# Kernel optimization log

Hardware: AMD Instinct MI355X
Metric: run time of the kernel (lower is better)

The kernel has to match this reference:

```python
import jax, jax.numpy as jnp
import numpy as np

D = 512
HEADS, DIM_HEAD, LANDMARKS, PINV_ITERS = 8, 64, 256, 6
CONV_K = 33  # residual depthwise conv kernel over sequence dim


def _ln(x, g, b, eps=1e-5):
    mu = x.mean(-1, keepdims=True)
    var = ((x - mu) ** 2).mean(-1, keepdims=True)
    return (x - mu) / jnp.sqrt(var + eps) * g + b


def _moe(x, gw, gb, f1w, f1b, l1g, l1b, f2w, f2b, l2g, l2b, k):
    # Dense grouped-expert evaluation (same math as per-token dispatch in torch source).
    scores = x @ gw + gb                               # [B,N,E]
    topk_s, topk_i = jax.lax.top_k(scores, k)          # [B,N,k]
    h = jnp.einsum('bnd,edh->benh', x, f1w) + f1b[None, :, None, :]
    h = jax.nn.relu(_ln(h, l1g[None, :, None, :], l1b[None, :, None, :]))
    o = jnp.einsum('benh,ehd->bend', h, f2w) + f2b[None, :, None, :]
    o = _ln(o, l2g[None, :, None, :], l2b[None, :, None, :])  # [B,E,N,D]
    o = jnp.take_along_axis(jnp.swapaxes(o, 1, 2), topk_i[..., None], axis=2)  # [B,N,k,D]
    w = jax.nn.softmax(topk_s, axis=-1)[..., None]
    return (w * o).sum(axis=2) + x


def _pinv(x, iters):
    # Moore-Penrose iterative pseudoinverse (lucidrains nystrom-attention)
    col = jnp.abs(x).sum(-1).max()
    row = jnp.abs(x).sum(-2).max()
    z = jnp.swapaxes(x, -1, -2) / (col * row)
    I = jnp.eye(x.shape[-1], dtype=x.dtype)
    for _ in range(iters):
        xz = x @ z
        z = 0.25 * z @ (13 * I - xz @ (15 * I - xz @ (7 * I - xz)))
    return z


def _nystrom(x, qkv_w, out_w, out_b, conv_w):
    b, n, _ = x.shape
    m, h, dh = LANDMARKS, HEADS, DIM_HEAD
    pad = (m - n % m) % m
    x = jnp.pad(x, ((0, 0), (pad, 0), (0, 0)))  # pad at FRONT, as in source
    npd = n + pad
    qkv = x @ qkv_w                              # [b, npd, 3*h*dh]
    q, k, v = [t.reshape(b, npd, h, dh).transpose(0, 2, 1, 3) for t in jnp.split(qkv, 3, axis=-1)]
    q = q * dh ** -0.5
    l = npd // m
    q_l = q.reshape(b, h, m, l, dh).mean(3)      # landmark means
    k_l = k.reshape(b, h, m, l, dh).mean(3)
    attn1 = jax.nn.softmax(jnp.einsum('bhid,bhjd->bhij', q, k_l), -1)    # [b,h,npd,m]
    attn2 = jax.nn.softmax(jnp.einsum('bhid,bhjd->bhij', q_l, k_l), -1)  # [b,h,m,m]
    attn3 = jax.nn.softmax(jnp.einsum('bhid,bhjd->bhij', q_l, k), -1)    # [b,h,m,npd]
    out = (attn1 @ _pinv(attn2, PINV_ITERS)) @ (attn3 @ v)               # [b,h,npd,dh]
    res = jax.lax.conv_general_dilated(
        v, conv_w, (1, 1), [(CONV_K // 2, CONV_K // 2), (0, 0)],
        dimension_numbers=('NCHW', 'OIHW', 'NCHW'), feature_group_count=h)
    out = out + res
    out = out.transpose(0, 2, 1, 3).reshape(b, npd, h * dh)
    out = out @ out_w + out_b
    return out[:, -n:]


def setup_inputs() -> dict:
    key = jax.random.key(0)
    ks = iter(jax.random.split(key, 64))
    def rn(shape, s=0.02):
        return jax.random.normal(next(ks), shape, jnp.float32) * s
    inp = {'features': jax.random.normal(next(ks), (4, 6000, D), jnp.float32)}
    inp['cls_token'] = rn((1, 1, D), 1e-6)
    def moe_params(pfx, E):
        inp[pfx + '_gate_w'] = rn((D, E)); inp[pfx + '_gate_b'] = jnp.zeros((E,), jnp.float32)
        inp[pfx + '_fc1_w'] = rn((E, D, D)); inp[pfx + '_fc1_b'] = jnp.zeros((E, D), jnp.float32)
        inp[pfx + '_ln1_g'] = jnp.ones((E, D), jnp.float32); inp[pfx + '_ln1_b'] = jnp.zeros((E, D), jnp.float32)
        inp[pfx + '_fc2_w'] = rn((E, D, D)); inp[pfx + '_fc2_b'] = jnp.zeros((E, D), jnp.float32)
        inp[pfx + '_ln2_g'] = jnp.ones((E, D), jnp.float32); inp[pfx + '_ln2_b'] = jnp.zeros((E, D), jnp.float32)
    moe_params('moe1', 2)
    moe_params('moe2', 4)
    def layer_params(pfx):
        inp[pfx + '_norm_g'] = jnp.ones((D,), jnp.float32); inp[pfx + '_norm_b'] = jnp.zeros((D,), jnp.float32)
        inp[pfx + '_qkv_w'] = rn((D, 3 * HEADS * DIM_HEAD))
        inp[pfx + '_out_w'] = rn((HEADS * DIM_HEAD, D)); inp[pfx + '_out_b'] = jnp.zeros((D,), jnp.float32)
        inp[pfx + '_conv_w'] = rn((HEADS, 1, CONV_K, 1))
    layer_params('l1')
    layer_params('l2')
    return inp


def reference(features, cls_token,
              moe1_gate_w, moe1_gate_b, moe1_fc1_w, moe1_fc1_b, moe1_ln1_g, moe1_ln1_b, moe1_fc2_w, moe1_fc2_b, moe1_ln2_g, moe1_ln2_b,
              moe2_gate_w, moe2_gate_b, moe2_fc1_w, moe2_fc1_b, moe2_ln1_g, moe2_ln1_b, moe2_fc2_w, moe2_fc2_b, moe2_ln2_g, moe2_ln2_b,
              l1_norm_g, l1_norm_b, l1_qkv_w, l1_out_w, l1_out_b, l1_conv_w,
              l2_norm_g, l2_norm_b, l2_qkv_w, l2_out_w, l2_out_b, l2_conv_w):
    B, N, _ = features.shape
    _H = int(np.ceil(np.sqrt(N)))
    add = _H * _H - N
    h = jnp.concatenate([features, features[:, :add]], axis=1)      # square pad by wrap
    h = jnp.concatenate([jnp.broadcast_to(cls_token, (B, 1, D)), h], axis=1)
    h = _moe(h, moe1_gate_w, moe1_gate_b, moe1_fc1_w, moe1_fc1_b, moe1_ln1_g, moe1_ln1_b, moe1_fc2_w, moe1_fc2_b, moe1_ln2_g, moe1_ln2_b, k=1)
    h = h + _nystrom(_ln(h, l1_norm_g, l1_norm_b), l1_qkv_w, l1_out_w, l1_out_b, l1_conv_w)
    h = _moe(h, moe2_gate_w, moe2_gate_b, moe2_fc1_w, moe2_fc1_b, moe2_ln1_g, moe2_ln1_b, moe2_fc2_w, moe2_fc2_b, moe2_ln2_g, moe2_ln2_b, k=2)
    h = h + _nystrom(_ln(h, l2_norm_g, l2_norm_b), l2_qkv_w, l2_out_w, l2_out_b, l2_conv_w)
    return (h[:, 0], h[:, 1:])
```

## Files before the change

### kernel.cpp

```cpp
#include <hip/hip_runtime.h>
#include <hip/hip_bf16.h>

constexpr int BATCH = 4;
constexpr int NTOK  = 6085;
constexpr int BN_TOK = BATCH * NTOK;
constexpr int NPD   = 6144;
constexpr int RPAD  = BATCH * NPD;
constexpr int DMODEL = 512;
constexpr int NH = 8, DH = 64;
constexpr int NBH = BATCH * NH;
constexpr int LGRP = NPD / 256;
constexpr int PAD_FRONT = 59;
constexpr int CONVK = 33;
constexpr int NCH = 8;

typedef __attribute__((ext_vector_type(8))) short short8v;
typedef __attribute__((ext_vector_type(4))) float f32x4;

__device__ __forceinline__ unsigned short f2bf(float f) {
  unsigned u = __float_as_uint(f);
  u += 0x7FFF + ((u >> 16) & 1);
  return (unsigned short)(u >> 16);
}
__device__ __forceinline__ float bf2f(unsigned short h) {
  return __uint_as_float((unsigned)h << 16);
}


__global__ void k_build_h(const float* __restrict__ feat, const float* __restrict__ cls,
                          float* __restrict__ H) {
  size_t total = (size_t)BN_TOK * DMODEL;
  for (size_t idx = (size_t)blockIdx.x * blockDim.x + threadIdx.x; idx < total;
       idx += (size_t)gridDim.x * blockDim.x) {
    int d = (int)(idx & 511);
    size_t tok = idx >> 9;
    int b = (int)(tok / NTOK), n = (int)(tok % NTOK);
    float v;
    if (n == 0) v = cls[d];
    else {
      int i = n - 1; if (i >= 6000) i -= 6000;
      v = feat[((size_t)b * 6000 + i) * DMODEL + d];
    }
    H[idx] = v;
  }
}

__global__ void k_diag_fill(float* __restrict__ out, size_t n, float val) {
  for (size_t i = (size_t)blockIdx.x * blockDim.x + threadIdx.x; i < n;
       i += (size_t)gridDim.x * blockDim.x)
    out[i] = val;
}

__global__ __launch_bounds__(256) void k_wconv(const float* __restrict__ W, int ldb,
    unsigned short* __restrict__ hi, unsigned short* __restrict__ lo) {
  __shared__ unsigned short Th[64][80], Tl[64][80];
  int bk = blockIdx.y * 64, bn = blockIdx.x * 64;
  int t = threadIdx.x;
  int kr = t >> 2, cq = (t & 3) * 16;
  const float* src = W + (size_t)(bk + kr) * ldb + bn + cq;
  #pragma unroll
  for (int q = 0; q < 4; ++q) {
    float4 v = *(const float4*)(src + q * 4);
    float vs[4] = {v.x, v.y, v.z, v.w};
    #pragma unroll
    for (int e = 0; e < 4; ++e) {
      int n = cq + q * 4 + e;
      unsigned short h = f2bf(vs[e]);
      Th[n][kr] = h;
      Tl[n][kr] = f2bf(vs[e] - bf2f(h));
    }
  }
  __syncthreads();
  int nr = t >> 2, kq = (t & 3) * 16;
  size_t o = (size_t)(bn + nr) * 512 + bk + kq;
  *(short8v*)&hi[o]     = *(const short8v*)&Th[nr][kq];
  *(short8v*)&hi[o + 8] = *(const short8v*)&Th[nr][kq + 8];
  *(short8v*)&lo[o]     = *(const short8v*)&Tl[nr][kq];
  *(short8v*)&lo[o + 8] = *(const short8v*)&Tl[nr][kq + 8];
}

__global__ __launch_bounds__(256) void k_gemm_mfma(const float* __restrict__ A,
    const unsigned short* __restrict__ BtH, const unsigned short* __restrict__ BtL,
    const float* __restrict__ bias, float* __restrict__ C,
    int M, int lda, int ldc, float alpha, int omode, unsigned short* __restrict__ Clo)
{
  __shared__ unsigned short AsH[128][40], AsL[128][40];
  __shared__ unsigned short BsH[128][40], BsL[128][40];
  int bm = blockIdx.y * 128, bn = blockIdx.x * 128;
  int tid = threadIdx.x;
  int wave = tid >> 6, lane = tid & 63;
  int mo = (wave >> 1) * 64, no = (wave & 1) * 64;
  int r16 = lane & 15, g = lane >> 4;
  f32x4 acc[4][4] = {};
  int srow = tid >> 1, shalf = (tid & 1) * 16;
  const float* aptr = A + (size_t)(bm + srow) * lda + shalf;
  bool avalid = (bm + srow) < M;
  const unsigned short* bhptr = BtH + (size_t)(bn + srow) * 512 + shalf;
  const unsigned short* blptr = BtL + (size_t)(bn + srow) * 512 + shalf;
  for (int k0 = 0; k0 < 512; k0 += 32) {
    unsigned short h8[16], l8[16];
    #pragma unroll
    for (int q = 0; q < 4; ++q) {
      float4 v = avalid ? *(const float4*)(aptr + k0 + q * 4) : make_float4(0.f, 0.f, 0.f, 0.f);
      float vs[4] = {v.x, v.y, v.z, v.w};
      #pragma unroll
      for (int e = 0; e < 4; ++e) {
        unsigned short hh = f2bf(vs[e]);
        h8[q * 4 + e] = hh;
        l8[q * 4 + e] = f2bf(vs[e] - bf2f(hh));
      }
    }
    *(short8v*)&AsH[srow][shalf]     = *(short8v*)&h8[0];
    *(short8v*)&AsH[srow][shalf + 8] = *(short8v*)&h8[8];
    *(short8v*)&AsL[srow][shalf]     = *(short8v*)&l8[0];
    *(short8v*)&AsL[srow][shalf + 8] = *(short8v*)&l8[8];
    *(short8v*)&BsH[srow][shalf]     = *(const short8v*)(bhptr + k0);
    *(short8v*)&BsH[srow][shalf + 8] = *(const short8v*)(bhptr + k0 + 8);
    *(short8v*)&BsL[srow][shalf]     = *(const short8v*)(blptr + k0);
    *(short8v*)&BsL[srow][shalf + 8] = *(const short8v*)(blptr + k0 + 8);
    __syncthreads();
    short8v ah[4], al[4], bh[4], bl[4];
    #pragma unroll
    for (int mt = 0; mt < 4; ++mt) {
      ah[mt] = *(const short8v*)&AsH[mo + mt * 16 + r16][g * 8];
      al[mt] = *(const short8v*)&AsL[mo + mt * 16 + r16][g * 8];
    }
    #pragma unroll
    for (int nt = 0; nt < 4; ++nt) {
      bh[nt] = *(const short8v*)&BsH[no + nt * 16 + r16][g * 8];
      bl[nt] = *(const short8v*)&BsL[no + nt * 16 + r16][g * 8];
    }
    #pragma unroll
    for (int mt = 0; mt < 4; ++mt)
      #pragma unroll
      for (int nt = 0; nt < 4; ++nt) {
        acc[mt][nt] = __builtin_amdgcn_mfma_f32_16x16x32_bf16(ah[mt], bh[nt], acc[mt][nt], 0, 0, 0);
        acc[mt][nt] = __builtin_amdgcn_mfma_f32_16x16x32_bf16(ah[mt], bl[nt], acc[mt][nt], 0, 0, 0);
        acc[mt][nt] = __builtin_amdgcn_mfma_f32_16x16x32_bf16(al[mt], bh[nt], acc[mt][nt], 0, 0, 0);
      }
    __syncthreads();
  }
  #pragma unroll
  for (int mt = 0; mt < 4; ++mt)
    #pragma unroll
    for (int nt = 0; nt < 4; ++nt)
      #pragma unroll
      for (int j = 0; j < 4; ++j) {
        int gr = bm + mo + mt * 16 + g * 4 + j;
        int gc = bn + no + nt * 16 + r16;
        if (gr >= M) continue;
        float v = alpha * acc[mt][nt][j] + (bias ? bias[gc] : 0.f);
        if (omode == 0) {
          C[(size_t)gr * ldc + gc] = v;
        } else if (omode == 2) {
          int bb = gr / NPD, ii = gr % NPD;
          if (ii >= PAD_FRONT)
            C[((size_t)bb * NTOK + ii - PAD_FRONT) * 512 + gc] += v;
        } else if (omode == 3) {
          int bb = gr / NPD, ii = gr % NPD;
          int hh = gc >> 6, dd = gc & 63;
          C[(((size_t)bb * NH + hh) * NPD + ii) * 64 + dd] = v;
        } else {
          int bb = gr / NPD, ii = gr % NPD;
          int hh = gc >> 6, dd = gc & 63;
          size_t idx = (((size_t)bb * NH + hh) * NPD + ii) * 64 + dd;
          unsigned short hi = f2bf(v);
          ((unsigned short*)C)[idx] = hi;
          Clo[idx] = f2bf(v - bf2f(hi));
        }
      }
}

__global__ __launch_bounds__(256) void k_gemm_mfma2(const float* __restrict__ A,
    const float* __restrict__ Bt, float* __restrict__ C,
    float alpha, int omode, float cdiag, int premap, int nprod)
{
  __shared__ unsigned short AsH[128][40], AsL[128][40];
  __shared__ unsigned short BsH[128][40], BsL[128][40];
  size_t zo = (size_t)blockIdx.z * 65536;
  int bm = blockIdx.y * 128, bn = blockIdx.x * 128;
  int tid = threadIdx.x;
  int wave = tid >> 6, lane = tid & 63;
  int mo = (wave >> 1) * 64, no = (wave & 1) * 64;
  int r16 = lane & 15, g = lane >> 4;
  f32x4 acc[4][4] = {};
  int srow = tid >> 1, shalf = (tid & 1) * 16;
  int grow = bm + srow;
  int gn = bn + srow;
  for (int k0 = 0; k0 < 256; k0 += 32) {
    unsigned short h8[16], l8[16];
    #pragma unroll
    for (int q = 0; q < 4; ++q) {
      float4 v = *(const float4*)&A[zo + (size_t)grow * 256 + k0 + shalf + q * 4];
      float vs[4] = {v.x, v.y, v.z, v.w};
      #pragma unroll
      for (int e = 0; e < 4; ++e) {
        float a = vs[e];
        if (premap) a = ((grow == (k0 + shalf + q * 4 + e)) ? 7.f : 0.f) - a;
        unsigned short hh = f2bf(a);
        h8[q * 4 + e] = hh;
        l8[q * 4 + e] = (nprod == 3) ? f2bf(a - bf2f(hh)) : (unsigned short)0;
      }
    }
    *(short8v*)&AsH[srow][shalf]     = *(short8v*)&h8[0];
    *(short8v*)&AsH[srow][shalf + 8] = *(short8v*)&h8[8];
    *(short8v*)&AsL[srow][shalf]     = *(short8v*)&l8[0];
    *(short8v*)&AsL[srow][shalf + 8] = *(short8v*)&l8[8];
    #pragma unroll
    for (int q = 0; q < 4; ++q) {
      float4 v = *(const float4*)&Bt[zo + (size_t)gn * 256 + k0 + shalf + q * 4];
      float vs[4] = {v.x, v.y, v.z, v.w};
      #pragma unroll
      for (int e = 0; e < 4; ++e) {
        unsigned short hh = f2bf(vs[e]);
        h8[q * 4 + e] = hh;
        l8[q * 4 + e] = (nprod == 3) ? f2bf(vs[e] - bf2f(hh)) : (unsigned short)0;
      }
    }
    *(short8v*)&BsH[srow][shalf]     = *(short8v*)&h8[0];
    *(short8v*)&BsH[srow][shalf + 8] = *(short8v*)&h8[8];
    *(short8v*)&BsL[srow][shalf]     = *(short8v*)&l8[0];
    *(short8v*)&BsL[srow][shalf + 8] = *(short8v*)&l8[8];
    __syncthreads();
    short8v ah[4], al[4], bh[4], bl[4];
    #pragma unroll
    for (int mt = 0; mt < 4; ++mt) {
      ah[mt] = *(const short8v*)&AsH[mo + mt * 16 + r16][g * 8];
      al[mt] = *(const short8v*)&AsL[mo + mt * 16 + r16][g * 8];
    }
    #pragma unroll
    for (int nt = 0; nt < 4; ++nt) {
      bh[nt] = *(const short8v*)&BsH[no + nt * 16 + r16][g * 8];
      bl[nt] = *(const short8v*)&BsL[no + nt * 16 + r16][g * 8];
    }
    #pragma unroll
    for (int mt = 0; mt < 4; ++mt)
      #pragma unroll
      for (int nt = 0; nt < 4; ++nt) {
        acc[mt][nt] = __builtin_amdgcn_mfma_f32_16x16x32_bf16(ah[mt], bh[nt], acc[mt][nt], 0, 0, 0);
        if (nprod == 3) {
          acc[mt][nt] = __builtin_amdgcn_mfma_f32_16x16x32_bf16(ah[mt], bl[nt], acc[mt][nt], 0, 0, 0);
          acc[mt][nt] = __builtin_amdgcn_mfma_f32_16x16x32_bf16(al[mt], bh[nt], acc[mt][nt], 0, 0, 0);
        }
      }
    __syncthreads();
  }
  #pragma unroll
  for (int mt = 0; mt < 4; ++mt)
    #pragma unroll
    for (int nt = 0; nt < 4; ++nt)
      #pragma unroll
      for (int j = 0; j < 4; ++j) {
        int gr = bm + mo + mt * 16 + g * 4 + j;
        int gc = bn + no + nt * 16 + r16;
        float v;
        if (omode == 5) v = ((gr == gc) ? cdiag : 0.f) - acc[mt][nt][j];
        else            v = alpha * acc[mt][nt][j];
        C[zo + (size_t)gr * 256 + gc] = v;
      }
}

__global__ __launch_bounds__(256) void k_tpose(const float* __restrict__ in,
                                               float* __restrict__ out) {
  __shared__ float Ts[64][65];
  int bx = blockIdx.x * 64, by = blockIdx.y * 64;
  size_t zo = (size_t)blockIdx.z * 65536;
  int t = threadIdx.x;
  int r = t >> 4, c4 = (t & 15) * 4;
  #pragma unroll
  for (int u = 0; u < 4; ++u) {
    float4 v = *(const float4*)&in[zo + (size_t)(by + r + u * 16) * 256 + bx + c4];
    Ts[r + u * 16][c4 + 0] = v.x; Ts[r + u * 16][c4 + 1] = v.y;
    Ts[r + u * 16][c4 + 2] = v.z; Ts[r + u * 16][c4 + 3] = v.w;
  }
  __syncthreads();
  #pragma unroll
  for (int u = 0; u < 4; ++u) {
    int rr = r + u * 16;
    float4 v = make_float4(Ts[c4][rr], Ts[c4 + 1][rr], Ts[c4 + 2][rr], Ts[c4 + 3][rr]);
    *(float4*)&out[zo + (size_t)(bx + rr) * 256 + by + c4] = v;
  }
}

__global__ void k_y0(const float* __restrict__ A2, float* __restrict__ Y,
                     const unsigned int* __restrict__ sc) {
  float scale = 1.f / (__uint_as_float(sc[0]) * __uint_as_float(sc[1]));
  size_t total = (size_t)NBH * 65536;
  for (size_t idx = (size_t)blockIdx.x * blockDim.x + threadIdx.x; idx < total;
       idx += (size_t)gridDim.x * blockDim.x)
    Y[idx] = A2[idx] * scale;
}

__global__ void k_zinit(const float* __restrict__ A2, float* __restrict__ Z,
                        const unsigned int* __restrict__ sc) {
  float scale = 1.f / (__uint_as_float(sc[0]) * __uint_as_float(sc[1]));
  size_t total = (size_t)NBH * 65536;
  for (size_t idx = (size_t)blockIdx.x * blockDim.x + threadIdx.x; idx < total;
       idx += (size_t)gridDim.x * blockDim.x) {
    size_t bh = idx >> 16; int r = (int)((idx >> 8) & 255); int cc = (int)(idx & 255);
    Z[idx] = A2[(bh << 16) + (size_t)cc * 256 + r] * scale;
  }
}

__global__ __launch_bounds__(256) void k_gemm(const float* __restrict__ A,
    const float* __restrict__ B,
    const float* __restrict__ bias, float* __restrict__ C,
    int M, int N, int K, int lda, int ldb, int ldc,
    long long sA, long long sB, long long sC, float alpha, int omode, float cdiag)
{
  __shared__ float As[16][65];
  __shared__ float Bs[16][65];
  int z = blockIdx.z;
  A += (size_t)z * (size_t)sA;
  B += (size_t)z * (size_t)sB;
  int bm = blockIdx.y * 64, bn = blockIdx.x * 64;
  int tid = threadIdx.x;
  int tr = tid >> 4, tc = tid & 15;
  int ar = tid >> 2, aq = tid & 3;
  int br = tid >> 4, bq = tid & 15;
  float acc[4][4] = {};
  for (int k0 = 0; k0 < K; k0 += 16) {
    {
      int gr = bm + ar;
      float4 v = make_float4(0.f, 0.f, 0.f, 0.f);
      if (gr < M) v = *(const float4*)&A[(size_t)gr * lda + k0 + aq * 4];
      As[aq * 4 + 0][ar] = v.x; As[aq * 4 + 1][ar] = v.y;
      As[aq * 4 + 2][ar] = v.z; As[aq * 4 + 3][ar] = v.w;
    }
    {
      float4 v = *(const float4*)&B[(size_t)(k0 + br) * ldb + bn + bq * 4];
      Bs[br][bq * 4 + 0] = v.x; Bs[br][bq * 4 + 1] = v.y;
      Bs[br][bq * 4 + 2] = v.z; Bs[br][bq * 4 + 3] = v.w;
    }
    __syncthreads();
    #pragma unroll
    for (int kk = 0; kk < 16; ++kk) {
      float a[4], bv[4];
      #pragma unroll
      for (int i = 0; i < 4; ++i) a[i] = As[kk][tr * 4 + i];
      #pragma unroll
      for (int j = 0; j < 4; ++j) bv[j] = Bs[kk][tc * 4 + j];
      #pragma unroll
      for (int i = 0; i < 4; ++i)
        #pragma unroll
        for (int j = 0; j < 4; ++j) acc[i][j] += a[i] * bv[j];
    }
    __syncthreads();
  }
  #pragma unroll
  for (int i = 0; i < 4; ++i) {
    int gr = bm + tr * 4 + i;
    if (gr >= M) continue;
    #pragma unroll
    for (int j = 0; j < 4; ++j) {
      int gc = bn + tc * 4 + j;
      float v;
      if (omode == 5) {
        v = ((gr == gc) ? cdiag : 0.f) - acc[i][j];
      } else {
        v = alpha * acc[i][j] + (bias ? bias[gc] : 0.f);
      }
      C[(size_t)z * (size_t)sC + (size_t)gr * ldc + gc] = v;
    }
  }
}

__global__ void k_gate(const float* __restrict__ X, const float* __restrict__ gw,
                       const float* __restrict__ gb, float* __restrict__ WT, int E, int k) {
  int tok = blockIdx.x; int lane = threadIdx.x;
  const float* x = X + (size_t)tok * DMODEL;
  float s[4] = {0.f, 0.f, 0.f, 0.f};
  for (int d = lane; d < DMODEL; d += 64) {
    float xv = x[d];
    for (int e = 0; e < E; ++e) s[e] += xv * gw[(size_t)d * E + e];
  }
  #pragma unroll
  for (int off = 32; off; off >>= 1) {
    #pragma unroll
    for (int e = 0; e < 4; ++e) s[e] += __shfl_down(s[e], off);
  }
  if (lane == 0) {
    for (int e = 0; e < E; ++e) s[e] += gb[e];
    float w[4] = {0.f, 0.f, 0.f, 0.f};
    int i1 = 0;
    for (int e = 1; e < E; ++e) if (s[e] > s[i1]) i1 = e;
    if (k == 1) {
      w[i1] = 1.f;
    } else {
      int i2 = -1;
      for (int e = 0; e < E; ++e) { if (e == i1) continue; if (i2 < 0 || s[e] > s[i2]) i2 = e; }
      float e2 = expf(s[i2] - s[i1]);
      float zz = 1.f + e2;
      w[i1] = 1.f / zz; w[i2] = e2 / zz;
    }
    #pragma unroll
    for (int e = 0; e < 4; ++e) WT[(size_t)tok * 4 + e] = w[e];
  }
}

__device__ __forceinline__ void wave_ln_stats(const float* x, int lane, float& mu, float& rstd) {
  float s = 0.f, q = 0.f;
  #pragma unroll
  for (int j = 0; j < 8; ++j) { float v = x[lane + 64 * j]; s += v; q += v * v; }
  #pragma unroll
  for (int off = 32; off; off >>= 1) { s += __shfl_xor(s, off); q += __shfl_xor(q, off); }
  mu = s * (1.f / 512.f);
  float var = q * (1.f / 512.f) - mu * mu;
  rstd = rsqrtf(var + 1e-5f);
}

__global__ void k_ln_relu(float* __restrict__ T, const float* __restrict__ g,
                          const float* __restrict__ b) {
  int row = blockIdx.x; int lane = threadIdx.x;
  float* x = T + (size_t)row * 512;
  float mu, rstd; wave_ln_stats(x, lane, mu, rstd);
  #pragma unroll
  for (int j = 0; j < 8; ++j) {
    int d = lane + 64 * j;
    float v = (x[d] - mu) * rstd * g[d] + b[d];
    x[d] = fmaxf(v, 0.f);
  }
}

__global__ void k_ln_waccum(const float* __restrict__ T, float* __restrict__ H,
                            const float* __restrict__ g, const float* __restrict__ b,
                            const float* __restrict__ WT, int e) {
  int row = blockIdx.x;
  float w = WT[(size_t)row * 4 + e];
  if (w == 0.f) return;
  int lane = threadIdx.x;
  const float* x = T + (size_t)row * 512;
  float mu, rstd; wave_ln_stats(x, lane, mu, rstd);
  float* h = H + (size_t)row * 512;
  #pragma unroll
  for (int j = 0; j < 8; ++j) {
    int d = lane + 64 * j;
    h[d] += w * ((x[d] - mu) * rstd * g[d] + b[d]);
  }
}

__global__ void k_ln_pad(const float* __restrict__ H, float* __restrict__ XLn,
                         const float* __restrict__ g, const float* __restrict__ b) {
  int row = blockIdx.x; int lane = threadIdx.x;
  int bb = row / NPD, i = row % NPD;
  float* y = XLn + (size_t)row * 512;
  if (i < PAD_FRONT) {
    #pragma unroll
    for (int j = 0; j < 8; ++j) y[lane + 64 * j] = 0.f;
    return;
  }
  const float* x = H + ((size_t)bb * NTOK + (i - PAD_FRONT)) * 512;
  float mu, rstd; wave_ln_stats(x, lane, mu, rstd);
  #pragma unroll
  for (int j = 0; j < 8; ++j) {
    int d = lane + 64 * j;
    y[d] = (x[d] - mu) * rstd * g[d] + b[d];
  }
}

__global__ void k_xmean(const float* __restrict__ XLn, float* __restrict__ Xm) {
  int z = blockIdx.x;
  int c = threadIdx.x;
  int b = z >> 8, jm = z & 255;
  const float* base = XLn + ((size_t)b * NPD + jm * LGRP) * 512 + c;
  float s = 0.f;
  #pragma unroll
  for (int t = 0; t < LGRP; ++t) s += base[(size_t)t * 512];
  Xm[(size_t)z * 512 + c] = s * (1.f / LGRP);
}

__global__ __launch_bounds__(256) void k_attn2(const float* __restrict__ QL,
                                               const float* __restrict__ KL,
                                               float* __restrict__ A2) {
  int z = blockIdx.x; int bh = z >> 8, j = z & 255;
  int b = bh >> 3, h = bh & 7;
  int t = threadIdx.x;
  __shared__ float q[64]; __shared__ float red[256];
  __shared__ float mshare, sshare;
  if (t < 64) q[t] = QL[((size_t)b * 256 + j) * 512 + h * 64 + t];
  __syncthreads();
  const float* kl = KL + ((size_t)b * 256 + t) * 512 + h * 64;
  float s = 0.f;
  #pragma unroll
  for (int d = 0; d < 64; ++d) s += q[d] * kl[d];
  red[t] = s; __syncthreads();
  for (int st = 128; st; st >>= 1) { if (t < st) red[t] = fmaxf(red[t], red[t + st]); __syncthreads(); }
  if (t == 0) mshare = red[0];
  __syncthreads();
  float e = expf(s - mshare);
  red[t] = e; __syncthreads();
  for (int st = 128; st; st >>= 1) { if (t < st) red[t] += red[t + st]; __syncthreads(); }
  if (t == 0) sshare = red[0];
  __syncthreads();
  A2[((size_t)bh * 256 + j) * 256 + t] = e / sshare;
}

__global__ __launch_bounds__(256) void k_pinv_scalars(const float* __restrict__ A2,
                                                      unsigned int* __restrict__ sc) {
  int bh = blockIdx.x; int t = threadIdx.x;
  const float* A = A2 + (size_t)bh * 65536;
  float rowsum = 0.f, colsum = 0.f;
  for (int jj = 0; jj < 256; ++jj) {
    rowsum += fabsf(A[(size_t)t * 256 + jj]);
    colsum += fabsf(A[(size_t)jj * 256 + t]);
  }
  __shared__ float sh[256];
  sh[t] = rowsum; __syncthreads();
  for (int s = 128; s; s >>= 1) { if (t < s) sh[t] = fmaxf(sh[t], sh[t + s]); __syncthreads(); }
  if (t == 0) atomicMax(&sc[0], __float_as_uint(sh[0]));
  __syncthreads();
  sh[t] = colsum; __syncthreads();
  for (int s = 128; s; s >>= 1) { if (t < s) sh[t] = fmaxf(sh[t], sh[t + s]); __syncthreads(); }
  if (t == 0) atomicMax(&sc[1], __float_as_uint(sh[0]));
}

__global__ __launch_bounds__(256) void k_vtpose(const unsigned short* __restrict__ VrH,
    const unsigned short* __restrict__ VrL,
    unsigned short* __restrict__ VtH, unsigned short* __restrict__ VtL) {
  __shared__ unsigned short TH[64][72], TL[64][72];
  int i0 = blockIdx.x * 64, bh = blockIdx.y;
  int t = threadIdx.x;
  const unsigned short* sH = VrH + ((size_t)bh * NPD + i0) * 64;
  const unsigned short* sL = VrL + ((size_t)bh * NPD + i0) * 64;
  #pragma unroll
  for (int u = 0; u < 2; ++u) {
    int idx = t + 256 * u;
    int r = idx >> 3, c8 = (idx & 7) * 8;
    *(short8v*)&TH[r][c8] = *(const short8v*)&sH[idx * 8];
    *(short8v*)&TL[r][c8] = *(const short8v*)&sL[idx * 8];
  }
  __syncthreads();
  #pragma unroll
  for (int u = 0; u < 2; ++u) {
    int idx = t + 256 * u;
    int d = idx >> 3, c8 = (idx & 7) * 8;
    unsigned short h8[8], l8[8];
    #pragma unroll
    for (int e = 0; e < 8; ++e) { h8[e] = TH[c8 + e][d]; l8[e] = TL[c8 + e][d]; }
    *(short8v*)&VtH[((size_t)bh * 64 + d) * NPD + i0 + c8] = *(short8v*)&h8[0];
    *(short8v*)&VtL[((size_t)bh * 64 + d) * NPD + i0 + c8] = *(short8v*)&l8[0];
  }
}

__global__ void k_cvt_kl(const float* __restrict__ KL, unsigned short* __restrict__ KH,
                         unsigned short* __restrict__ KLo) {
  int idx = blockIdx.x * 256 + threadIdx.x;
  int bh = idx >> 14, j = (idx >> 6) & 255, d = idx & 63;
  int b = bh >> 3, h = bh & 7;
  float v = KL[((size_t)b * 256 + j) * 512 + h * 64 + d];
  unsigned short hi = f2bf(v);
  KH[idx] = hi; KLo[idx] = f2bf(v - bf2f(hi));
}

__global__ void k_cvt_w2t(const float* __restrict__ W2b, unsigned short* __restrict__ WH,
                          unsigned short* __restrict__ WL) {
  int idx = blockIdx.x * 256 + threadIdx.x;
  int bh = idx >> 14, d = (idx >> 8) & 63, j = idx & 255;
  float v = W2b[((size_t)bh * 256 + j) * 64 + d];
  unsigned short hi = f2bf(v);
  WH[idx] = hi; WL[idx] = f2bf(v - bf2f(hi));
}

__global__ __launch_bounds__(256) void k_flash_pre(
    const float* __restrict__ Qp, long long Qsb, long long Qsh, int Qsr,
    const unsigned short* __restrict__ KHg, const unsigned short* __restrict__ KLg,
    long long Ksbh,
    const unsigned short* __restrict__ VtHg, const unsigned short* __restrict__ VtLg,
    long long Vsbh, int Vrow,
    float* __restrict__ Op, long long Osb, long long Osh, int Osr,
    float* __restrict__ Opart, float* __restrict__ ML,
    int tiles_per_chunk, int mode)
{
  int jt = blockIdx.x, bh = blockIdx.y, ch = blockIdx.z;
  int b = bh >> 3, h = bh & 7;
  const float* Qb = Qp + (size_t)b * Qsb + (size_t)h * Qsh;
  const unsigned short* KbH = KHg + (size_t)bh * Ksbh;
  const unsigned short* KbL = KLg + (size_t)bh * Ksbh;
  const unsigned short* VbH = VtHg + (size_t)bh * Vsbh;
  const unsigned short* VbL = VtLg + (size_t)bh * Vsbh;
  int tid = threadIdx.x;
  int wave = tid >> 6, lane = tid & 63;
  int r16 = lane & 15, g = lane >> 4;
  int q0 = jt * 64 + wave * 16;

  __shared__ unsigned short KsH[64][72], KsL[64][72];
  __shared__ unsigned short VtH[64][72], VtL[64][72];

  short8v qh[2], ql[2];
  #pragma unroll
  for (int kk = 0; kk < 2; ++kk) {
    const float* qr = Qb + (size_t)(q0 + r16) * Qsr + kk * 32 + g * 8;
    float4 v0 = *(const float4*)qr;
    float4 v1 = *(const float4*)(qr + 4);
    float vs[8] = {v0.x, v0.y, v0.z, v0.w, v1.x, v1.y, v1.z, v1.w};
    unsigned short hh[8], llo[8];
    #pragma unroll
    for (int e = 0; e < 8; ++e) {
      hh[e] = f2bf(vs[e]); llo[e] = f2bf(vs[e] - bf2f(hh[e]));
    }
    qh[kk] = *(short8v*)&hh[0];
    ql[kk] = *(short8v*)&llo[0];
  }

  f32x4 O4[4] = {};
  float m[4], lsum[4];
  #pragma unroll
  for (int j = 0; j < 4; ++j) { m[j] = -1e30f; lsum[j] = 0.f; }

  int t0 = ch * tiles_per_chunk;
  for (int tt = t0; tt < t0 + tiles_per_chunk; ++tt) {
    int key0 = tt * 64;
    __syncthreads();
    {
      const unsigned short* ksrcH = KbH + (size_t)key0 * 64;
      const unsigned short* ksrcL = KbL + (size_t)key0 * 64;
      #pragma unroll
      for (int u = 0; u < 2; ++u) {
        int idx = tid + 256 * u;
        int r = idx >> 3, c8 = (idx & 7) * 8;
        *(short8v*)&KsH[r][c8] = *(const short8v*)&ksrcH[idx * 8];
        *(short8v*)&KsL[r][c8] = *(const short8v*)&ksrcL[idx * 8];
      }
      const unsigned short* vsrcH = VbH + key0;
      const unsigned short* vsrcL = VbL + key0;
      #pragma unroll
      for (int u = 0; u < 2; ++u) {
        int idx = tid + 256 * u;
        int d = idx >> 3, c8 = (idx & 7) * 8;
        *(short8v*)&VtH[d][c8] = *(const short8v*)&vsrcH[(size_t)d * Vrow + c8];
        *(short8v*)&VtL[d][c8] = *(const short8v*)&vsrcL[(size_t)d * Vrow + c8];
      }
    }
    __syncthreads();
    f32x4 S[4] = {};
    #pragma unroll
    for (int kk = 0; kk < 2; ++kk)
      #pragma unroll
      for (int nt = 0; nt < 4; ++nt) {
        short8v kh = *(const short8v*)&KsH[nt * 16 + r16][kk * 32 + g * 8];
        short8v kl = *(const short8v*)&KsL[nt * 16 + r16][kk * 32 + g * 8];
        S[nt] = __builtin_amdgcn_mfma_f32_16x16x32_bf16(qh[kk], kh, S[nt], 0, 0, 0);
        S[nt] = __builtin_amdgcn_mfma_f32_16x16x32_bf16(qh[kk], kl, S[nt], 0, 0, 0);
        S[nt] = __builtin_amdgcn_mfma_f32_16x16x32_bf16(ql[kk], kh, S[nt], 0, 0, 0);
      }
    float tmax[4];
    #pragma unroll
    for (int j = 0; j < 4; ++j)
      tmax[j] = fmaxf(fmaxf(S[0][j], S[1][j]), fmaxf(S[2][j], S[3][j]));
    #pragma unroll
    for (int off = 8; off; off >>= 1)
      #pragma unroll
      for (int j = 0; j < 4; ++j) tmax[j] = fmaxf(tmax[j], __shfl_xor(tmax[j], off));
    float corr[4];
    #pragma unroll
    for (int j = 0; j < 4; ++j) {
      float mn = fmaxf(m[j], tmax[j]);
      corr[j] = expf(m[j] - mn);
      m[j] = mn;
    }
    __syncthreads();
    float tl[4] = {0.f, 0.f, 0.f, 0.f};
    #pragma unroll
    for (int nt = 0; nt < 4; ++nt)
      #pragma unroll
      for (int j = 0; j < 4; ++j) {
        float p = expf(S[nt][j] - m[j]);
        tl[j] += p;
        KsH[wave * 16 + g * 4 + j][nt * 16 + r16] = f2bf(p);
      }
    #pragma unroll
    for (int off = 8; off; off >>= 1)
      #pragma unroll
      for (int j = 0; j < 4; ++j) tl[j] += __shfl_xor(tl[j], off);
    #pragma unroll
    for (int j = 0; j < 4; ++j) lsum[j] = lsum[j] * corr[j] + tl[j];
    #pragma unroll
    for (int nt = 0; nt < 4; ++nt)
      #pragma unroll
      for (int j = 0; j < 4; ++j) O4[nt][j] *= corr[j];
    #pragma unroll
    for (int kk = 0; kk < 2; ++kk) {
      short8v ph = *(const short8v*)&KsH[wave * 16 + r16][kk * 32 + g * 8];
      #pragma unroll
      for (int nt = 0; nt < 4; ++nt) {
        short8v vh = *(const short8v*)&VtH[nt * 16 + r16][kk * 32 + g * 8];
        short8v vl = *(const short8v*)&VtL[nt * 16 + r16][kk * 32 + g * 8];
        O4[nt] = __builtin_amdgcn_mfma_f32_16x16x32_bf16(ph, vh, O4[nt], 0, 0, 0);
        O4[nt] = __builtin_amdgcn_mfma_f32_16x16x32_bf16(ph, vl, O4[nt], 0, 0, 0);
      }
    }
  }
  if (mode == 0) {
    float* Ob = Op + (size_t)b * Osb + (size_t)h * Osh;
    float inv[4];
    #pragma unroll
    for (int j = 0; j < 4; ++j) inv[j] = 1.f / lsum[j];
    #pragma unroll
    for (int nt = 0; nt < 4; ++nt)
      #pragma unroll
      for (int j = 0; j < 4; ++j)
        Ob[(size_t)(q0 + g * 4 + j) * Osr + nt * 16 + r16] = O4[nt][j] * inv[j];
  } else {
    #pragma unroll
    for (int j = 0; j < 4; ++j) {
      size_t rowbase = ((size_t)ch * NBH + bh) * 256 + q0 + g * 4 + j;
      #pragma unroll
      for (int nt = 0; nt < 4; ++nt)
        Opart[rowbase * 64 + nt * 16 + r16] = O4[nt][j];
      if (r16 == 0) { ML[rowbase * 2] = m[j]; ML[rowbase * 2 + 1] = lsum[j]; }
    }
  }
}

__global__ __launch_bounds__(256) void k_flash_comb(const float* __restrict__ Opart,
                                                    const float* __restrict__ ML,
                                                    float* __restrict__ A3V) {
  int jt = blockIdx.x, bh = blockIdx.y;
  int t = threadIdx.x;
  int jr = t >> 4, q16 = t & 15;
  int row = jt * 16 + jr;
  float mv[NCH], lv[NCH];
  float M = -1e30f;
  #pragma unroll
  for (int ch = 0; ch < NCH; ++ch) {
    size_t base = (((size_t)ch * NBH + bh) * 256 + row);
    mv[ch] = ML[base * 2]; lv[ch] = ML[base * 2 + 1];
    M = fmaxf(M, mv[ch]);
  }
  float L = 0.f;
  float4 O = make_float4(0.f, 0.f, 0.f, 0.f);
  #pragma unroll
  for (int ch = 0; ch < NCH; ++ch) {
    float c = expf(mv[ch] - M);
    L += c * lv[ch];
    size_t base = (((size_t)ch * NBH + bh) * 256 + row);
    float4 o = *(const float4*)&Opart[base * 64 + q16 * 4];
    O.x += c * o.x; O.y += c * o.y; O.z += c * o.z; O.w += c * o.w;
  }
  float inv = 1.f / L;
  *(float4*)&A3V[((size_t)bh * 256 + row) * 64 + q16 * 4] =
      make_float4(O.x * inv, O.y * inv, O.z * inv, O.w * inv);
}

__global__ __launch_bounds__(256) void k_conv_add(const unsigned short* __restrict__ VtHg,
    const unsigned short* __restrict__ VtLg, const float* __restrict__ cw,
    float* __restrict__ out) {
  int it = blockIdx.x, bh = blockIdx.y;
  int b = bh >> 3, h = bh & 7;
  int i0 = it * 128;
  int t = threadIdx.x;
  __shared__ float Vs[64][161];
  const unsigned short* vh = VtHg + (size_t)bh * 64 * NPD;
  const unsigned short* vl = VtLg + (size_t)bh * 64 * NPD;
  for (int u = 0; u < 40; ++u) {
    int idx = t + 256 * u;
    int d = idx / 160, ii = idx - d * 160;
    int gi = i0 - 16 + ii;
    float v = 0.f;
    if (gi >= 0 && gi < NPD) {
      size_t a = (size_t)d * NPD + gi;
      v = bf2f(vh[a]) + bf2f(vl[a]);
    }
    Vs[d][ii] = v;
  }
  __syncthreads();
  float w[CONVK];
  #pragma unroll
  for (int p = 0; p < CONVK; ++p) w[p] = cw[h * CONVK + p];
  int rgrp = t >> 6, d = t & 63;
  for (int r = rgrp * 32; r < rgrp * 32 + 32; ++r) {
    float acc = 0.f;
    #pragma unroll
    for (int p = 0; p < CONVK; ++p) acc += w[p] * Vs[d][r + p];
    out[((size_t)b * NPD + i0 + r) * 512 + h * 64 + d] += acc;
  }
}

__global__ void k_out_write(const float* __restrict__ H, float* __restrict__ out) {
  size_t n0 = (size_t)BATCH * 512;
  size_t total = n0 + (size_t)BATCH * (NTOK - 1) * 512;
  for (size_t idx = (size_t)blockIdx.x * blockDim.x + threadIdx.x; idx < total;
       idx += (size_t)gridDim.x * blockDim.x) {
    float v;
    if (idx < n0) {
      int b = (int)(idx >> 9); int d = (int)(idx & 511);
      v = H[((size_t)b * NTOK) * 512 + d];
    } else {
      size_t r = idx - n0;
      size_t bj = r >> 9; int d = (int)(r & 511);
      int b = (int)(bj / (NTOK - 1)); int j = (int)(bj % (NTOK - 1));
      v = H[((size_t)b * NTOK + 1 + j) * 512 + d];
    }
    out[idx] = v;
  }
}


extern "C" void kernel_launch(void* const* d_in, const int* in_sizes, int n_in,
                              void* d_out, int out_size, void* d_ws, size_t ws_size,
                              hipStream_t stream) {
  (void)in_sizes; (void)n_in;

  const float* feat = (const float*)d_in[0];
  const float* cls  = (const float*)d_in[1];
  const float* m1_gw = (const float*)d_in[2];  const float* m1_gb = (const float*)d_in[3];
  const float* m1_f1w = (const float*)d_in[4]; const float* m1_f1b = (const float*)d_in[5];
  const float* m1_l1g = (const float*)d_in[6]; const float* m1_l1b = (const float*)d_in[7];
  const float* m1_f2w = (const float*)d_in[8]; const float* m1_f2b = (const float*)d_in[9];
  const float* m1_l2g = (const float*)d_in[10]; const float* m1_l2b = (const float*)d_in[11];
  const float* m2_gw = (const float*)d_in[12]; const float* m2_gb = (const float*)d_in[13];
  const float* m2_f1w = (const float*)d_in[14]; const float* m2_f1b = (const float*)d_in[15];
  const float* m2_l1g = (const float*)d_in[16]; const float* m2_l1b = (const float*)d_in[17];
  const float* m2_f2w = (const float*)d_in[18]; const float* m2_f2b = (const float*)d_in[19];
  const float* m2_l2g = (const float*)d_in[20]; const float* m2_l2b = (const float*)d_in[21];
  const float* l1_ng = (const float*)d_in[22]; const float* l1_nb = (const float*)d_in[23];
  const float* l1_qkvw = (const float*)d_in[24]; const float* l1_outw = (const float*)d_in[25];
  const float* l1_outb = (const float*)d_in[26]; const float* l1_convw = (const float*)d_in[27];
  const float* l2_ng = (const float*)d_in[28]; const float* l2_nb = (const float*)d_in[29];
  const float* l2_qkvw = (const float*)d_in[30]; const float* l2_outw = (const float*)d_in[31];
  const float* l2_outb = (const float*)d_in[32]; const float* l2_convw = (const float*)d_in[33];

  constexpr size_t SZ_H    = (size_t)BN_TOK * 512;
  constexpr size_t SZ_ROW  = (size_t)RPAD * 512;
  float* W = (float*)d_ws;
  float* H  = W;
  float* WT = W + SZ_H;
  unsigned int* SC = (unsigned int*)(W + SZ_H + 97360);
  float* pool = W + SZ_H + 97360 + 16;

  float* R2 = pool;
  float* R3 = pool + SZ_ROW;
  float* R4 = pool + 2 * SZ_ROW;
  float* SMALL = pool + 3 * SZ_ROW;
  float* Xm  = SMALL;
  float* QL  = SMALL + 524288;
  float* KL  = SMALL + 1048576;
  float* A2  = SMALL + 1572864;
  float* Zb  = SMALL + 3670016;
  float* XZp = SMALL + 5767168;
  float* Wa  = SMALL + 7864320;
  float* Wb  = SMALL + 9961472;
  float* A3V = SMALL + 12058624;
  float* W2b = SMALL + 12582912;
  size_t total_f = (SZ_H + 97360 + 16) + 3 * SZ_ROW + 13107200;
  if (total_f * 4 > ws_size) {
    k_diag_fill<<<2048, 256, 0, stream>>>((float*)d_out, (size_t)out_size,
                                          (float)(ws_size >> 20));
    return;
  }

  k_build_h<<<2048, 256, 0, stream>>>(feat, cls, H);

  auto run_moe = [&](const float* gw, const float* gb, const float* f1w, const float* f1b,
                     const float* l1g, const float* l1b, const float* f2w, const float* f2b,
                     const float* l2g, const float* l2b, int E, int k) {
    float* T1 = R2; float* T2 = R3; float* Xsnap = R4;
    unsigned short* BtHi = (unsigned short*)A2;
    unsigned short* BtLo = (unsigned short*)(A2 + 131072);
    hipMemcpyAsync(Xsnap, H, SZ_H * 4, hipMemcpyDeviceToDevice, stream);
    k_gate<<<BN_TOK, 64, 0, stream>>>(H, gw, gb, WT, E, k);
    dim3 g(4, (BN_TOK + 127) / 128, 1);
    for (int e = 0; e < E; ++e) {
      k_wconv<<<dim3(8, 8), 256, 0, stream>>>(f1w + (size_t)e * 262144, 512, BtHi, BtLo);
      k_gemm_mfma<<<g, 256, 0, stream>>>(Xsnap, BtHi, BtLo, f1b + e * 512, T1,
          BN_TOK, 512, 512, 1.f, 0, nullptr);
      k_ln_relu<<<BN_TOK, 64, 0, stream>>>(T1, l1g + e * 512, l1b + e * 512);
      k_wconv<<<dim3(8, 8), 256, 0, stream>>>(f2w + (size_t)e * 262144, 512, BtHi, BtLo);
      k_gemm_mfma<<<g, 256, 0, stream>>>(T1, BtHi, BtLo, f2b + e * 512, T2,
          BN_TOK, 512, 512, 1.f, 0, nullptr);
      k_ln_waccum<<<BN_TOK, 64, 0, stream>>>(T2, H, l2g + e * 512, l2b + e * 512, WT, e);
    }
  };

  auto run_attn = [&](const float* ng, const float* nb, const float* qkvw, const float* outw,
                      const float* outb, const float* convw) {
    float* XLn = R2; float* AttnO = R2;
    float* Qb = R3;
    unsigned short* VrH = (unsigned short*)R3;
    unsigned short* VrL = VrH + 12582912;
    unsigned short* KH  = (unsigned short*)R3;
    unsigned short* KLo = KH + 12582912;
    unsigned short* VtH = (unsigned short*)R4;
    unsigned short* VtL = VtH + 12582912;
    k_ln_pad<<<RPAD, 64, 0, stream>>>(H, XLn, ng, nb);
    k_xmean<<<BATCH * 256, 512, 0, stream>>>(XLn, Xm);
    k_gemm<<<dim3(8, 16, 1), 256, 0, stream>>>(Xm, qkvw, nullptr, QL,
        1024, 512, 512, 512, 1536, 512, 0, 0, 0, 0.125f, 0, 0.f);
    k_gemm<<<dim3(8, 16, 1), 256, 0, stream>>>(Xm, qkvw + 512, nullptr, KL,
        1024, 512, 512, 512, 1536, 512, 0, 0, 0, 1.f, 0, 0.f);
    k_attn2<<<NBH * 256, 256, 0, stream>>>(QL, KL, A2);
    hipMemsetAsync(SC, 0, 8, stream);
    k_pinv_scalars<<<NBH, 256, 0, stream>>>(A2, SC);
    k_y0<<<2048, 256, 0, stream>>>(A2, Zb, SC);
    k_zinit<<<2048, 256, 0, stream>>>(A2, Wb, SC);
    float* Y = Zb; float* Z = Wb; float* F1 = XZp; float* F2 = Wa;
    dim3 gq(2, 2, NBH);
    for (int it = 0; it < 6; ++it) {
      int np = (it < 4) ? 1 : 3;
      k_gemm_mfma2<<<gq, 256, 0, stream>>>(A2, Y, F1, 1.f, 0, 0.f, 0, np);
      k_tpose<<<dim3(4, 4, NBH), 256, 0, stream>>>(F1, F2);
      k_gemm_mfma2<<<gq, 256, 0, stream>>>(F2, F1, Y, 1.f, 5, 15.f, 1, np);
      k_gemm_mfma2<<<gq, 256, 0, stream>>>(Y, F1, F2, 1.f, 5, 13.f, 0, np);
      k_gemm_mfma2<<<gq, 256, 0, stream>>>(Z, F2, F1, 0.25f, 0, 0.f, 0, np);
      float* tz = Z; Z = F1; F1 = tz;
      if (it < 5)
        k_tpose<<<dim3(4, 4, NBH), 256, 0, stream>>>(Z, Y);
    }
    unsigned short* KLH = (unsigned short*)A2;
    unsigned short* KLL = KLH + 524288;
    unsigned short* W2tH = KLH + 1048576;
    unsigned short* W2tL = KLH + 1572864;
    k_cvt_kl<<<2048, 256, 0, stream>>>(KL, KLH, KLL);
    unsigned short* BtQH = (unsigned short*)Wa;
    unsigned short* BtQL = BtQH + 786432;
    k_wconv<<<dim3(24, 8), 256, 0, stream>>>(qkvw, 1536, BtQH, BtQL);
    dim3 gr(4, (RPAD + 127) / 128, 1);
    k_gemm_mfma<<<gr, 256, 0, stream>>>(XLn, BtQH + 1024 * 512, BtQL + 1024 * 512, nullptr,
        (float*)VrH, RPAD, 512, 512, 1.f, 6, VrL);
    k_vtpose<<<dim3(NPD / 64, NBH), 256, 0, stream>>>(VrH, VrL, VtH, VtL);
    k_gemm_mfma<<<gr, 256, 0, stream>>>(XLn, BtQH + 512 * 512, BtQL + 512 * 512, nullptr,
        (float*)KH, RPAD, 512, 512, 1.f, 6, KLo);
    k_flash_pre<<<dim3(4, NBH, NCH), 256, 0, stream>>>(
        QL, 131072LL, 64LL, 512,
        KH, KLo, (long long)NPD * 64,
        VtH, VtL, (long long)64 * NPD, NPD,
        nullptr, 0, 0, 0, Zb, Xm, NPD / (64 * NCH), 1);
    k_flash_comb<<<dim3(16, NBH), 256, 0, stream>>>(Zb, Xm, A3V);
    k_gemm<<<dim3(1, 4, NBH), 256, 0, stream>>>(Z, A3V, nullptr, W2b,
        256, 64, 256, 256, 64, 64, 65536, 16384, 16384, 1.f, 0, 0.f);
    k_cvt_w2t<<<2048, 256, 0, stream>>>(W2b, W2tH, W2tL);
    k_gemm_mfma<<<gr, 256, 0, stream>>>(XLn, BtQH, BtQL, nullptr,
        Qb, RPAD, 512, 512, 0.125f, 0, nullptr);
    k_flash_pre<<<dim3(NPD / 64, NBH, 1), 256, 0, stream>>>(
        Qb, (long long)NPD * 512, 64LL, 512,
        KLH, KLL, 16384LL,
        W2tH, W2tL, 16384LL, 256,
        AttnO, (long long)NPD * 512, 64LL, 512,
        nullptr, nullptr, 4, 0);
    k_conv_add<<<dim3(NPD / 128, NBH), 256, 0, stream>>>(VtH, VtL, convw, AttnO);
    unsigned short* BtOH = (unsigned short*)Wa;
    unsigned short* BtOL = BtOH + 262144;
    k_wconv<<<dim3(8, 8), 256, 0, stream>>>(outw, 512, BtOH, BtOL);
    k_gemm_mfma<<<gr, 256, 0, stream>>>(AttnO, BtOH, BtOL, outb,
        H, RPAD, 512, 512, 1.f, 2, nullptr);
  };

  run_moe(m1_gw, m1_gb, m1_f1w, m1_f1b, m1_l1g, m1_l1b, m1_f2w, m1_f2b, m1_l2g, m1_l2b, 2, 1);
  run_attn(l1_ng, l1_nb, l1_qkvw, l1_outw, l1_outb, l1_convw);
  run_moe(m2_gw, m2_gb, m2_f1w, m2_f1b, m2_l1g, m2_l1b, m2_f2w, m2_f2b, m2_l2g, m2_l2b, 4, 2);
  run_attn(l2_ng, l2_nb, l2_qkvw, l2_outw, l2_outb, l2_convw);

  k_out_write<<<2048, 256, 0, stream>>>(H, (float*)d_out);
}
```

Baseline: 3.807 ms.

## Prefetch next GEMM k-tile into registers and remap workgroups per XCD

The split-bf16 MFMA GEMM now issues global loads for the next 32-wide k slice into registers right after the barrier, so they overlap the MFMA work on the current tile. Workgroup IDs are also remapped so that consecutive output tiles land on the same XCD, which is meant to improve L2 reuse of the A and B tiles. The prefetch raises register pressure and may lower occupancy.

```diff
diff --git a/kernel.cpp b/kernel.cpp
--- a/kernel.cpp
+++ b/kernel.cpp
@@ -86,7 +86,13 @@
 {
   __shared__ unsigned short AsH[128][40], AsL[128][40];
   __shared__ unsigned short BsH[128][40], BsL[128][40];
-  int bm = blockIdx.y * 128, bn = blockIdx.x * 128;
+  int nwg = gridDim.x * gridDim.y;
+  int wid = blockIdx.y * gridDim.x + blockIdx.x;
+  int qq = nwg >> 3, rr = nwg & 7;
+  int xcd = wid & 7, pos = wid >> 3;
+  int Lid = (xcd < rr ? xcd * (qq + 1) : rr * (qq + 1) + (xcd - rr) * qq) + pos;
+  int bn = (Lid % gridDim.x) * 128;
+  int bm = (Lid / gridDim.x) * 128;
   int tid = threadIdx.x;
   int wave = tid >> 6, lane = tid & 63;
   int mo = (wave >> 1) * 64, no = (wave & 1) * 64;
@@ -97,28 +103,46 @@
   bool avalid = (bm + srow) < M;
   const unsigned short* bhptr = BtH + (size_t)(bn + srow) * 512 + shalf;
   const unsigned short* blptr = BtL + (size_t)(bn + srow) * 512 + shalf;
+  float4 z4 = make_float4(0.f, 0.f, 0.f, 0.f);
+  float4 ra0 = avalid ? *(const float4*)(aptr + 0)  : z4;
+  float4 ra1 = avalid ? *(const float4*)(aptr + 4)  : z4;
+  float4 ra2 = avalid ? *(const float4*)(aptr + 8)  : z4;
+  float4 ra3 = avalid ? *(const float4*)(aptr + 12) : z4;
+  short8v rbh0 = *(const short8v*)(bhptr + 0);
+  short8v rbh1 = *(const short8v*)(bhptr + 8);
+  short8v rbl0 = *(const short8v*)(blptr + 0);
+  short8v rbl1 = *(const short8v*)(blptr + 8);
   for (int k0 = 0; k0 < 512; k0 += 32) {
+    float va[16];
+    *(float4*)&va[0]  = ra0; *(float4*)&va[4]  = ra1;
+    *(float4*)&va[8]  = ra2; *(float4*)&va[12] = ra3;
     unsigned short h8[16], l8[16];
     #pragma unroll
-    for (int q = 0; q < 4; ++q) {
-      float4 v = avalid ? *(const float4*)(aptr + k0 + q * 4) : make_float4(0.f, 0.f, 0.f, 0.f);
-      float vs[4] = {v.x, v.y, v.z, v.w};
-      #pragma unroll
-      for (int e = 0; e < 4; ++e) {
-        unsigned short hh = f2bf(vs[e]);
-        h8[q * 4 + e] = hh;
-        l8[q * 4 + e] = f2bf(vs[e] - bf2f(hh));
-      }
+    for (int e = 0; e < 16; ++e) {
+      unsigned short hh = f2bf(va[e]);
+      h8[e] = hh;
+      l8[e] = f2bf(va[e] - bf2f(hh));
     }
     *(short8v*)&AsH[srow][shalf]     = *(short8v*)&h8[0];
     *(short8v*)&AsH[srow][shalf + 8] = *(short8v*)&h8[8];
     *(short8v*)&AsL[srow][shalf]     = *(short8v*)&l8[0];
     *(short8v*)&AsL[srow][shalf + 8] = *(short8v*)&l8[8];
-    *(short8v*)&BsH[srow][shalf]     = *(const short8v*)(bhptr + k0);
-    *(short8v*)&BsH[srow][shalf + 8] = *(const short8v*)(bhptr + k0 + 8);
-    *(short8v*)&BsL[srow][shalf]     = *(const short8v*)(blptr + k0);
-    *(short8v*)&BsL[srow][shalf + 8] = *(const short8v*)(blptr + k0 + 8);
+    *(short8v*)&BsH[srow][shalf]     = rbh0;
+    *(short8v*)&BsH[srow][shalf + 8] = rbh1;
+    *(short8v*)&BsL[srow][shalf]     = rbl0;
+    *(short8v*)&BsL[srow][shalf + 8] = rbl1;
     __syncthreads();
+    if (k0 + 32 < 512) {
+      int kn = k0 + 32;
+      ra0 = avalid ? *(const float4*)(aptr + kn)      : z4;
+      ra1 = avalid ? *(const float4*)(aptr + kn + 4)  : z4;
+      ra2 = avalid ? *(const float4*)(aptr + kn + 8)  : z4;
+      ra3 = avalid ? *(const float4*)(aptr + kn + 12) : z4;
+      rbh0 = *(const short8v*)(bhptr + kn);
+      rbh1 = *(const short8v*)(bhptr + kn + 8);
+      rbl0 = *(const short8v*)(blptr + kn);
+      rbl1 = *(const short8v*)(blptr + kn + 8);
+    }
     short8v ah[4], al[4], bh[4], bl[4];
     #pragma unroll
     for (int mt = 0; mt < 4; ++mt) {
```

After: 4.185 ms. 1.1x slower.
